# Kernel optimization log

Measured on AMD Instinct MI355X. Metric: run time of the kernel, lower is better.

The kernel has to match this reference:

```python
import jax, jax.numpy as jnp
import numpy as np

B, N, C, H, MLP = 4, 1024, 768, 6, 2304  # num_heads = C // 128
D = C // H  # head dim = 128


def setup_inputs() -> dict:
    key = jax.random.key(0)
    ks = iter(jax.random.split(key, 64))
    def nrm(shape, s=0.02):
        return jax.random.normal(next(ks), shape, jnp.float32) * s
    inp = {}
    for nm in ("queries", "change_emb", "imageA_emb", "imageB_emb", "pe"):
        inp[nm] = jax.random.normal(next(ks), (B, N, C), jnp.float32)
    # three Attention modules: self-attn (1), change->ABC cross (2), imageAB->change cross (3)
    for i in (1, 2, 3):
        for p in ("q", "k", "v", "o"):
            inp[f"w{p}{i}"] = nrm((C, C))       # stored [in, out]; y = x @ W + b
            inp[f"b{p}{i}"] = jnp.zeros((C,), jnp.float32)
    for i in (1, 2, 3):
        inp[f"ln{i}_w"] = jnp.ones((C,), jnp.float32)
        inp[f"ln{i}_b"] = jnp.zeros((C,), jnp.float32)
    inp["mlp_w1"] = nrm((C, MLP)); inp["mlp_b1"] = jnp.zeros((MLP,), jnp.float32)
    inp["mlp_w2"] = nrm((MLP, C)); inp["mlp_b2"] = jnp.zeros((C,), jnp.float32)
    inp["flag_a"] = nrm((C,)); inp["flag_b"] = nrm((C,)); inp["flag_c"] = nrm((C,))
    return inp


def _ln(x, w, b, eps=1e-5):
    m = jnp.mean(x, -1, keepdims=True)
    v = jnp.var(x, -1, keepdims=True)
    return (x - m) * jax.lax.rsqrt(v + eps) * w + b


def _mha(q, k, v, wq, bq, wk, bk, wv, bv, wo, bo):
    b, nq, _ = q.shape
    qh = (q @ wq + bq).reshape(b, nq, H, D)
    kh = (k @ wk + bk).reshape(b, k.shape[1], H, D)
    vh = (v @ wv + bv).reshape(b, v.shape[1], H, D)
    scores = jnp.einsum('bqhd,bkhd->bhqk', qh, kh) / np.float32(np.sqrt(D))
    attn = jax.nn.softmax(scores, axis=-1)
    out = jnp.einsum('bhqk,bkhd->bqhd', attn, vh).reshape(b, nq, H * D)
    return out @ wo + bo


def reference(queries, change_emb, imageA_emb, imageB_emb, pe,
              wq1, bq1, wk1, bk1, wv1, bv1, wo1, bo1,
              wq2, bq2, wk2, bk2, wv2, bv2, wo2, bo2,
              wq3, bq3, wk3, bk3, wv3, bv3, wo3, bo3,
              ln1_w, ln1_b, ln2_w, ln2_b, ln3_w, ln3_b,
              mlp_w1, mlp_b1, mlp_w2, mlp_b2,
              flag_a, flag_b, flag_c):
    # --- self attention on change queries (skip_first_layer_add=False) ---
    q0 = queries + change_emb
    a = _mha(q0 + pe, q0 + pe, q0, wq1, bq1, wk1, bk1, wv1, bv1, wo1, bo1)
    q1 = _ln(q0 + a, ln1_w, ln1_b)
    # --- cross attention: change -> [imageA, imageB, change] ---
    qf = q1 + pe + flag_c
    k2 = jnp.concatenate((imageA_emb + pe + flag_a,
                          imageB_emb + pe + flag_b,
                          q1 + pe + flag_c), axis=1)
    v2 = jnp.concatenate((imageA_emb, imageB_emb, q1), axis=1)
    a = _mha(qf, k2, v2, wq2, bq2, wk2, bk2, wv2, bv2, wo2, bo2)
    q2 = _ln(q1 + a, ln2_w, ln2_b)
    # --- MLP (exact GELU, as nn.GELU default) ---
    mlp_out = jax.nn.gelu(q2 @ mlp_w1 + mlp_b1, approximate=False) @ mlp_w2 + mlp_b2
    q3 = _ln(q2 + mlp_out, ln3_w, ln3_b)
    change_out = q3
    # --- cross attention: [imageA; imageB] -> [image; change], batched along dim 0 ---
    qa = imageA_emb + pe + flag_a
    qb = imageB_emb + pe + flag_b
    ka = jnp.concatenate((imageA_emb + pe + flag_a, q3 + pe + flag_c), axis=1)
    kb = jnp.concatenate((imageB_emb + pe + flag_b, q3 + pe + flag_c), axis=1)
    va = jnp.concatenate((imageA_emb, q3), axis=1)
    vb = jnp.concatenate((imageB_emb, q3), axis=1)
    q = jnp.concatenate((qa, qb), axis=0)   # [2B, N, C]
    k = jnp.concatenate((ka, kb), axis=0)   # [2B, 2N, C]
    v = jnp.concatenate((va, vb), axis=0)
    a = _mha(q, k, v, wq3, bq3, wk3, bk3, wv3, bv3, wo3, bo3)
    q = q + a
    image_A_refined, image_B_refined = jnp.split(q, 2, axis=0)
    return (image_A_refined, image_B_refined, change_out)
```

## Files before the change

kernel.cpp:

```cpp
#include <hip/hip_runtime.h>
#include <hip/hip_bf16.h>
#include <math.h>

typedef short bf16x8 __attribute__((ext_vector_type(8)));
typedef float f32x4 __attribute__((ext_vector_type(4)));
using bf16_t = __hip_bfloat16;

#define DEV static __device__ __forceinline__

DEV unsigned short f2bu(float x) {
  bf16_t h = __float2bfloat16(x);
  unsigned short u;
  __builtin_memcpy(&u, &h, 2);
  return u;
}
DEV void st4(bf16_t* p, float a, float b, float c, float d) {
  ushort4 u;
  u.x = f2bu(a); u.y = f2bu(b); u.z = f2bu(c); u.w = f2bu(d);
  *reinterpret_cast<ushort4*>(p) = u;
}

DEV void async_copy16(const bf16_t* g, bf16_t* lds) {
  __builtin_amdgcn_global_load_lds(
      (const __attribute__((address_space(1))) unsigned int*)g,
      (__attribute__((address_space(3))) unsigned int*)lds, 16, 0, 0);
}

struct WPack {
  const float* s[12];
  bf16_t* d[12];
  float scale0;
};

__global__ __launch_bounds__(256) void k_wt12(WPack pk) {
  __shared__ float tile[32][33];
  int z = blockIdx.z;
  const float* W = pk.s[z];
  bf16_t* WT = pk.d[z];
  float scale = (z == 0) ? pk.scale0 : 1.0f;
  int i0 = blockIdx.x * 32;
  int o0 = blockIdx.y * 32;
  int tx = threadIdx.x & 31, ty = threadIdx.x >> 5;
  for (int r = ty; r < 32; r += 8)
    tile[r][tx] = W[(size_t)(i0 + r) * 768 + (o0 + tx)];
  __syncthreads();
  for (int r = ty; r < 32; r += 8)
    WT[(size_t)(o0 + r) * 768 + (i0 + tx)] = __float2bfloat16(tile[tx][r] * scale);
}

__global__ __launch_bounds__(256) void k_wt(const float* __restrict__ W, bf16_t* __restrict__ WT,
                                            int in_dim, int out_dim) {
  __shared__ float tile[32][33];
  int i0 = blockIdx.x * 32;
  int o0 = blockIdx.y * 32;
  int tx = threadIdx.x & 31, ty = threadIdx.x >> 5;
  for (int r = ty; r < 32; r += 8)
    tile[r][tx] = W[(size_t)(i0 + r) * out_dim + (o0 + tx)];
  __syncthreads();
  for (int r = ty; r < 32; r += 8)
    WT[(size_t)(o0 + r) * in_dim + (i0 + tx)] = __float2bfloat16(tile[tx][r]);
}

__global__ __launch_bounds__(256) void k_bqk(const float* __restrict__ bq, const float* __restrict__ bk,
                                             float* __restrict__ out, float qa) {
  int i = blockIdx.x * 256 + threadIdx.x;
  if (i < 768) out[i] = bq[i] * qa;
  else if (i < 1536) out[i] = bk[i - 768];
}

__global__ __launch_bounds__(256) void k_prep1(const float4* __restrict__ q, const float4* __restrict__ ce,
                                               const float4* __restrict__ pe,
                                               bf16_t* __restrict__ qpe_b, bf16_t* __restrict__ q0_b, int n4) {
  int i = blockIdx.x * 256 + threadIdx.x;
  if (i >= n4) return;
  float4 a = q[i], b = ce[i], p = pe[i];
  float sx = a.x + b.x, sy = a.y + b.y, sz = a.z + b.z, sw = a.w + b.w;
  st4(q0_b + 4 * (size_t)i, sx, sy, sz, sw);
  st4(qpe_b + 4 * (size_t)i, sx + p.x, sy + p.y, sz + p.z, sw + p.w);
}

__global__ __launch_bounds__(256) void k_buildqq(const float* __restrict__ imA, const float* __restrict__ imB,
                                                 const float* __restrict__ pe, const float* __restrict__ fa,
                                                 const float* __restrict__ fb, bf16_t* __restrict__ qq,
                                                 bf16_t* __restrict__ imAB) {
  int idx = blockIdx.x * 256 + threadIdx.x;
  int c4 = idx % 192; int rem = idx / 192;
  int n = rem & 1023; int bb = rem >> 10;
  int b = bb & 3, isB = bb >> 2;
  int c = c4 * 4;
  size_t tok = (size_t)(b * 1024 + n) * 768 + c;
  float4 s = *(const float4*)((isB ? imB : imA) + tok);
  float4 p = *(const float4*)(pe + tok);
  float4 f = *(const float4*)((isB ? fb : fa) + c);
  size_t o = (size_t)rem * 768 + c;
  st4(imAB + o, s.x, s.y, s.z, s.w);
  st4(qq + o, s.x + p.x + f.x, s.y + p.y + f.y, s.z + p.z + f.z, s.w + p.w + f.w);
}

struct FArgs {
  const bf16_t* Q; bf16_t* O;
  const bf16_t* Kp[3]; const bf16_t* Vp[3];
  int badd[3], bmask[3];
  int ldq, ldk;
  long qStrideB, oStrideB;
};

template<int NSEG>
__global__ __launch_bounds__(256, 3) void k_flash(FArgs fa) {
  const int z = blockIdx.y; const int b = z / 6, h = z % 6;
  const bf16_t* Qb = fa.Q + (size_t)b * fa.qStrideB + h * 128;
  bf16_t* Ob = fa.O + (size_t)b * fa.oStrideB + h * 128;
  const int q0 = blockIdx.x * 64;
  const int tid = threadIdx.x, lane = tid & 63, w = tid >> 6;
  const int g = lane >> 4, c = lane & 15;

  __shared__ bf16_t Ks[64][136];
  __shared__ bf16_t Vs[128][72];
  __shared__ bf16_t Ps[64][72];

  bf16x8 qf[4];
#pragma unroll
  for (int kk = 0; kk < 4; kk++)
    qf[kk] = *reinterpret_cast<const bf16x8*>(
        &Qb[(size_t)(q0 + w * 16 + c) * fa.ldq + kk * 32 + g * 8]);

  f32x4 oa[8];
  float m[4], l[4];
#pragma unroll
  for (int d = 0; d < 8; d++) { f32x4 zz = {0.f, 0.f, 0.f, 0.f}; oa[d] = zz; }
#pragma unroll
  for (int r = 0; r < 4; r++) { m[r] = -1.0e30f; l[r] = 0.f; }

  const int kr_ = tid >> 4, kc_ = (tid & 15) * 8;
  const int vr_ = tid >> 3, vc_ = (tid & 7) * 8;
  const int ldk = fa.ldk;

#pragma unroll
  for (int s = 0; s < NSEG; ++s) {
    const int bi = fa.badd[s] + (b & fa.bmask[s]);
    const bf16_t* Kb = fa.Kp[s] + (size_t)bi * 1024 * ldk + h * 128;
    const bf16_t* Vb = fa.Vp[s] + (size_t)(bi * 6 + h) * 128 * 1024;
    for (int t = 0; t < 16; ++t) {
      const int k0 = t << 6;
#pragma unroll
      for (int p = 0; p < 4; p++)
        *reinterpret_cast<uint4*>(&Ks[p * 16 + kr_][kc_]) =
            *reinterpret_cast<const uint4*>(&Kb[(size_t)(k0 + p * 16 + kr_) * ldk + kc_]);
#pragma unroll
      for (int p = 0; p < 4; p++)
        *reinterpret_cast<uint4*>(&Vs[p * 32 + vr_][vc_]) =
            *reinterpret_cast<const uint4*>(&Vb[(size_t)(p * 32 + vr_) * 1024 + k0 + vc_]);
      __syncthreads();

      f32x4 sx[4];
#pragma unroll
      for (int j = 0; j < 4; j++) { f32x4 zz = {0.f, 0.f, 0.f, 0.f}; sx[j] = zz; }
      __builtin_amdgcn_s_setprio(1);
#pragma unroll
      for (int kk = 0; kk < 4; kk++)
#pragma unroll
        for (int j = 0; j < 4; j++) {
          bf16x8 kf = *reinterpret_cast<const bf16x8*>(&Ks[j * 16 + c][kk * 32 + g * 8]);
          sx[j] = __builtin_amdgcn_mfma_f32_16x16x32_bf16(qf[kk], kf, sx[j], 0, 0, 0);
        }
      __builtin_amdgcn_s_setprio(0);

      float tl[4];
#pragma unroll
      for (int r = 0; r < 4; r++)
        tl[r] = fmaxf(fmaxf(sx[0][r], sx[1][r]), fmaxf(sx[2][r], sx[3][r]));
      float ex = fmaxf(fmaxf(tl[0] - m[0], tl[1] - m[1]), fmaxf(tl[2] - m[2], tl[3] - m[3]));
      if (__any(ex > 8.0f)) {
#pragma unroll
        for (int r = 0; r < 4; r++) {
          float tv = tl[r];
          tv = fmaxf(tv, __shfl_xor(tv, 1));
          tv = fmaxf(tv, __shfl_xor(tv, 2));
          tv = fmaxf(tv, __shfl_xor(tv, 4));
          tv = fmaxf(tv, __shfl_xor(tv, 8));
          float mn = fmaxf(m[r], tv);
          float f = exp2f(m[r] - mn);
          m[r] = mn;
          l[r] *= f;
#pragma unroll
          for (int d = 0; d < 8; d++) oa[d][r] *= f;
        }
      }
#pragma unroll
      for (int j = 0; j < 4; j++)
#pragma unroll
        for (int r = 0; r < 4; r++) {
          float p = exp2f(sx[j][r] - m[r]);
          l[r] += p;
          Ps[w * 16 + g * 4 + r][j * 16 + c] = __float2bfloat16(p);
        }

      __builtin_amdgcn_s_setprio(1);
#pragma unroll
      for (int kk = 0; kk < 2; kk++) {
        bf16x8 pf = *reinterpret_cast<const bf16x8*>(&Ps[w * 16 + c][kk * 32 + g * 8]);
#pragma unroll
        for (int d = 0; d < 8; d++) {
          bf16x8 vf = *reinterpret_cast<const bf16x8*>(&Vs[d * 16 + c][kk * 32 + g * 8]);
          oa[d] = __builtin_amdgcn_mfma_f32_16x16x32_bf16(pf, vf, oa[d], 0, 0, 0);
        }
      }
      __builtin_amdgcn_s_setprio(0);
      __syncthreads();
    }
  }

  float inv[4];
#pragma unroll
  for (int r = 0; r < 4; r++) {
    float t2 = l[r];
    t2 += __shfl_xor(t2, 1);
    t2 += __shfl_xor(t2, 2);
    t2 += __shfl_xor(t2, 4);
    t2 += __shfl_xor(t2, 8);
    inv[r] = 1.0f / t2;
  }
#pragma unroll
  for (int d = 0; d < 8; d++) {
    int col = d * 16 + c;
#pragma unroll
    for (int r = 0; r < 4; r++) {
      int row = q0 + w * 16 + g * 4 + r;
      Ob[(size_t)row * 768 + col] = __float2bfloat16(oa[d][r] * inv[r]);
    }
  }
}

__global__ __launch_bounds__(256) void k_ln(const float* __restrict__ X1, const float* __restrict__ X2,
                                            const float* __restrict__ A,
                                            const float* __restrict__ w, const float* __restrict__ bvec,
                                            float* __restrict__ outf, bf16_t* __restrict__ outb,
                                            const float* __restrict__ pe, const float* __restrict__ flag,
                                            bf16_t* __restrict__ outpf) {
  int row = blockIdx.x, tid = threadIdx.x;
  size_t base = (size_t)row * 768;
  float v0 = X1[base + tid] + A[base + tid];
  float v1 = X1[base + tid + 256] + A[base + tid + 256];
  float v2 = X1[base + tid + 512] + A[base + tid + 512];
  if (X2) {
    v0 += X2[base + tid]; v1 += X2[base + tid + 256]; v2 += X2[base + tid + 512];
  }
  float s = v0 + v1 + v2;
  for (int o = 32; o; o >>= 1) s += __shfl_xor(s, o);
  __shared__ float sm[8];
  int wv = tid >> 6, ln = tid & 63;
  if (ln == 0) sm[wv] = s;
  __syncthreads();
  s = sm[0] + sm[1] + sm[2] + sm[3];
  float mean = s * (1.0f / 768.0f);
  float d0 = v0 - mean, d1 = v1 - mean, d2 = v2 - mean;
  float ss = d0 * d0 + d1 * d1 + d2 * d2;
  for (int o = 32; o; o >>= 1) ss += __shfl_xor(ss, o);
  if (ln == 0) sm[4 + wv] = ss;
  __syncthreads();
  ss = sm[4] + sm[5] + sm[6] + sm[7];
  float rstd = rsqrtf(ss * (1.0f / 768.0f) + 1e-5f);
  float o0 = d0 * rstd * w[tid] + bvec[tid];
  float o1 = d1 * rstd * w[tid + 256] + bvec[tid + 256];
  float o2 = d2 * rstd * w[tid + 512] + bvec[tid + 512];
  outf[base + tid] = o0; outf[base + tid + 256] = o1; outf[base + tid + 512] = o2;
  if (outb) {
    outb[base + tid] = __float2bfloat16(o0);
    outb[base + tid + 256] = __float2bfloat16(o1);
    outb[base + tid + 512] = __float2bfloat16(o2);
  }
  if (outpf) {
    outpf[base + tid] = __float2bfloat16(o0 + pe[base + tid] + flag[tid]);
    outpf[base + tid + 256] = __float2bfloat16(o1 + pe[base + tid + 256] + flag[tid + 256]);
    outpf[base + tid + 512] = __float2bfloat16(o2 + pe[base + tid + 512] + flag[tid + 512]);
  }
}

struct GArgs {
  const bf16_t* X; const bf16_t* Wt; const float* bias; void* Out;
  const bf16_t* resid;
  int K, ldx, ldw, ldo, vNk, mode;
  float alpha;
};
struct GPack {
  GArgs a[7];
  int cum[7];
  int nx[7];
};

__global__ __launch_bounds__(256, 2) void k_gemmN(GPack pk) {
  GArgs a; int base, nx;
  {
    int idx = blockIdx.x;
    if (idx < pk.cum[0])      { a = pk.a[0]; base = 0;          nx = pk.nx[0]; }
    else if (idx < pk.cum[1]) { a = pk.a[1]; base = pk.cum[0];  nx = pk.nx[1]; }
    else if (idx < pk.cum[2]) { a = pk.a[2]; base = pk.cum[1];  nx = pk.nx[2]; }
    else if (idx < pk.cum[3]) { a = pk.a[3]; base = pk.cum[2];  nx = pk.nx[3]; }
    else if (idx < pk.cum[4]) { a = pk.a[4]; base = pk.cum[3];  nx = pk.nx[4]; }
    else if (idx < pk.cum[5]) { a = pk.a[5]; base = pk.cum[4];  nx = pk.nx[5]; }
    else                      { a = pk.a[6]; base = pk.cum[5];  nx = pk.nx[6]; }
  }
  int idx = blockIdx.x - base;
  const int brow = (idx / nx) * 128;
  const int bcol = (idx % nx) * 128;

  __shared__ bf16_t As[128 * 32];
  __shared__ bf16_t Bs[128 * 32];

  const int tid = threadIdx.x;
  const int lane = tid & 63;
  const int wave = tid >> 6;
  const int wr = wave >> 1;
  const int wc = wave & 1;

  f32x4 acc[4][4];
#pragma unroll
  for (int i = 0; i < 4; i++)
#pragma unroll
    for (int j = 0; j < 4; j++) {
      f32x4 zz = {0.f, 0.f, 0.f, 0.f};
      acc[i][j] = zz;
    }

  const int sr = lane >> 2;
  const int sc = (lane & 3) * 8;
  const int lrow = lane & 15;
  const int kch = (lane >> 4) * 8;

  const int nK = a.K >> 5;
  for (int kk = 0; kk < nK; ++kk) {
    const int k0 = kk << 5;
#pragma unroll
    for (int q = 0; q < 2; q++) {
      const int rows = wave * 32 + q * 16;
      async_copy16(a.X + (size_t)(brow + rows + sr) * a.ldx + k0 + sc, As + rows * 32);
      async_copy16(a.Wt + (size_t)(bcol + rows + sr) * a.ldw + k0 + sc, Bs + rows * 32);
    }
    __syncthreads();

    bf16x8 afr[4], bfr[4];
#pragma unroll
    for (int i = 0; i < 4; i++)
      afr[i] = *reinterpret_cast<const bf16x8*>(&As[(wr * 64 + i * 16 + lrow) * 32 + kch]);
#pragma unroll
    for (int j = 0; j < 4; j++)
      bfr[j] = *reinterpret_cast<const bf16x8*>(&Bs[(wc * 64 + j * 16 + lrow) * 32 + kch]);
#pragma unroll
    for (int i = 0; i < 4; i++)
#pragma unroll
      for (int j = 0; j < 4; j++)
        acc[i][j] = __builtin_amdgcn_mfma_f32_16x16x32_bf16(afr[i], bfr[j], acc[i][j], 0, 0, 0);
    __syncthreads();
  }

  const int lcol = lane & 15;
  const int lrow4 = (lane >> 4) * 4;

  if (a.mode == 2) {
    const int bi = brow / a.vNk;
    const int n0 = brow - bi * a.vNk;
#pragma unroll
    for (int i = 0; i < 4; i++) {
      int rloc = n0 + wr * 64 + i * 16 + lrow4;
#pragma unroll
      for (int j = 0; j < 4; j++) {
        int col = bcol + wc * 64 + j * 16 + lcol;
        int hh = col >> 7, dd = col & 127;
        float bv = a.bias[col];
        ushort4 u;
        u.x = f2bu(acc[i][j][0] + bv);
        u.y = f2bu(acc[i][j][1] + bv);
        u.z = f2bu(acc[i][j][2] + bv);
        u.w = f2bu(acc[i][j][3] + bv);
        bf16_t* dst = reinterpret_cast<bf16_t*>(a.Out) +
                      ((size_t)(bi * 6 + hh) * 128 + dd) * (size_t)a.vNk + rloc;
        *reinterpret_cast<ushort4*>(dst) = u;
      }
    }
  } else if (a.mode == 3) {
#pragma unroll
    for (int i = 0; i < 4; i++) {
      int row0 = brow + wr * 64 + i * 16 + lrow4;
#pragma unroll
      for (int j = 0; j < 4; j++) {
        int col = bcol + wc * 64 + j * 16 + lcol;
        float bv = a.bias[col];
#pragma unroll
        for (int r = 0; r < 4; r++) {
          size_t idx2 = (size_t)(row0 + r) * a.ldo + col;
          float rv = __bfloat162float(a.resid[(size_t)(row0 + r) * 768 + col]);
          reinterpret_cast<float*>(a.Out)[idx2] = acc[i][j][r] + bv + rv;
        }
      }
    }
  } else {
#pragma unroll
    for (int i = 0; i < 4; i++) {
      int row0 = brow + wr * 64 + i * 16 + lrow4;
#pragma unroll
      for (int j = 0; j < 4; j++) {
        int col = bcol + wc * 64 + j * 16 + lcol;
        float bv = a.bias[col];
#pragma unroll
        for (int r = 0; r < 4; r++)
          reinterpret_cast<bf16_t*>(a.Out)[(size_t)(row0 + r) * a.ldo + col] =
              __float2bfloat16((acc[i][j][r] + bv) * a.alpha);
      }
    }
  }
}

static inline void packN(hipStream_t st, const GArgs* as, const int* Ms, const int* Ns, int n) {
  GPack pk;
  int tot = 0;
  for (int i = 0; i < 7; ++i) {
    int j = i < n ? i : n - 1;
    pk.a[i] = as[j];
    pk.nx[i] = Ns[j] / 128;
    if (i < n) tot += (Ns[j] / 128) * (Ms[j] / 128);
    pk.cum[i] = tot;
  }
  k_gemmN<<<dim3(tot), 256, 0, st>>>(pk);
}

template<int OUTBF, int GELU>
__global__ __launch_bounds__(256, 2) void k_gemm(
    const bf16_t* __restrict__ X, const bf16_t* __restrict__ Wt,
    const float* __restrict__ bias, void* __restrict__ Out,
    int M, int Nout, int K, int ldx, int ldw, int ldo, float alpha) {
  const int brow = blockIdx.y * 128;
  const int bcol = blockIdx.x * 128;

  __shared__ bf16_t As[128 * 32];
  __shared__ bf16_t Bs[128 * 32];

  const int tid = threadIdx.x;
  const int lane = tid & 63;
  const int wave = tid >> 6;
  const int wr = wave >> 1;
  const int wc = wave & 1;

  f32x4 acc[4][4];
#pragma unroll
  for (int i = 0; i < 4; i++)
#pragma unroll
    for (int j = 0; j < 4; j++) {
      f32x4 zz = {0.f, 0.f, 0.f, 0.f};
      acc[i][j] = zz;
    }

  const int sr = lane >> 2;
  const int sc = (lane & 3) * 8;
  const int lrow = lane & 15;
  const int kch = (lane >> 4) * 8;

  const int nK = K >> 5;
  for (int kk = 0; kk < nK; ++kk) {
    const int k0 = kk << 5;
#pragma unroll
    for (int q = 0; q < 2; q++) {
      const int rows = wave * 32 + q * 16;
      async_copy16(X + (size_t)(brow + rows + sr) * ldx + k0 + sc, As + rows * 32);
      async_copy16(Wt + (size_t)(bcol + rows + sr) * ldw + k0 + sc, Bs + rows * 32);
    }
    __syncthreads();

    bf16x8 afr[4], bfr[4];
#pragma unroll
    for (int i = 0; i < 4; i++)
      afr[i] = *reinterpret_cast<const bf16x8*>(&As[(wr * 64 + i * 16 + lrow) * 32 + kch]);
#pragma unroll
    for (int j = 0; j < 4; j++)
      bfr[j] = *reinterpret_cast<const bf16x8*>(&Bs[(wc * 64 + j * 16 + lrow) * 32 + kch]);
#pragma unroll
    for (int i = 0; i < 4; i++)
#pragma unroll
      for (int j = 0; j < 4; j++)
        acc[i][j] = __builtin_amdgcn_mfma_f32_16x16x32_bf16(afr[i], bfr[j], acc[i][j], 0, 0, 0);
    __syncthreads();
  }

  const int lcol = lane & 15;
  const int lrow4 = (lane >> 4) * 4;

#pragma unroll
  for (int i = 0; i < 4; i++) {
    int row0 = brow + wr * 64 + i * 16 + lrow4;
#pragma unroll
    for (int j = 0; j < 4; j++) {
      int col = bcol + wc * 64 + j * 16 + lcol;
      float bv = bias ? bias[col] : 0.0f;
#pragma unroll
      for (int r = 0; r < 4; r++) {
        float v = (acc[i][j][r] + bv) * alpha;
        if (GELU) v = 0.5f * v * (1.0f + erff(v * 0.70710678118f));
        size_t idx = (size_t)(row0 + r) * ldo + col;
        if (OUTBF) reinterpret_cast<bf16_t*>(Out)[idx] = __float2bfloat16(v);
        else reinterpret_cast<float*>(Out)[idx] = v;
      }
    }
  }
}

static inline void gemm(hipStream_t st, const bf16_t* X, const bf16_t* Wt, const float* bias,
                        void* out, int outBf, int gelu, int M, int N, int K,
                        int ldx, int ldw, int ldo, float alpha = 1.0f) {
  dim3 g(N / 128, M / 128), blk(256);
  if (outBf) {
    if (gelu) k_gemm<1, 1><<<g, blk, 0, st>>>(X, Wt, bias, out, M, N, K, ldx, ldw, ldo, alpha);
    else      k_gemm<1, 0><<<g, blk, 0, st>>>(X, Wt, bias, out, M, N, K, ldx, ldw, ldo, alpha);
  } else      k_gemm<0, 0><<<g, blk, 0, st>>>(X, Wt, bias, out, M, N, K, ldx, ldw, ldo, alpha);
}

extern "C" void kernel_launch(void* const* d_in, const int* in_sizes, int n_in,
                              void* d_out, int out_size, void* d_ws, size_t ws_size,
                              hipStream_t stream) {
  (void)in_sizes; (void)n_in; (void)out_size; (void)ws_size;
  constexpr int B = 4, N = 1024, C = 768, Hh = 6, MLPD = 2304;
  constexpr size_t BNC = (size_t)B * N * C;
  constexpr size_t NC  = (size_t)N * C;
  const float qalpha = 0.08838834764831845f * 1.4426950408889634f;

  const float* queries = (const float*)d_in[0];
  const float* change  = (const float*)d_in[1];
  const float* imA     = (const float*)d_in[2];
  const float* imB     = (const float*)d_in[3];
  const float* pe      = (const float*)d_in[4];
  const float* bq1 = (const float*)d_in[6];  const float* bk1 = (const float*)d_in[8];
  const float* bv1 = (const float*)d_in[10]; const float* bo1 = (const float*)d_in[12];
  const float* bq2 = (const float*)d_in[14]; const float* bk2 = (const float*)d_in[16];
  const float* bv2 = (const float*)d_in[18]; const float* bo2 = (const float*)d_in[20];
  const float* bq3 = (const float*)d_in[22]; const float* bk3 = (const float*)d_in[24];
  const float* bv3 = (const float*)d_in[26]; const float* bo3 = (const float*)d_in[28];
  const float* ln1w = (const float*)d_in[29]; const float* ln1b = (const float*)d_in[30];
  const float* ln2w = (const float*)d_in[31]; const float* ln2b = (const float*)d_in[32];
  const float* ln3w = (const float*)d_in[33]; const float* ln3b = (const float*)d_in[34];
  const float* mb1 = (const float*)d_in[36]; const float* mb2 = (const float*)d_in[38];
  const float* fa = (const float*)d_in[39];
  const float* fb = (const float*)d_in[40];
  const float* fc = (const float*)d_in[41];

  char* base = (char*)d_ws;
  size_t off = 0;
  auto alloc = [&](size_t bytes) -> void* {
    void* p = base + off;
    off += (bytes + 255) & ~(size_t)255;
    return p;
  };

  bf16_t* WT[14];
  const int widx[14] = {5, 7, 9, 11, 13, 15, 17, 19, 21, 23, 25, 27, 35, 37};
  for (int i = 0; i < 12; i++) WT[i] = (bf16_t*)alloc((size_t)768 * 768 * 2);
  WT[12] = (bf16_t*)alloc((size_t)768 * 2304 * 2);
  WT[13] = (bf16_t*)alloc((size_t)2304 * 768 * 2);
  float* bqk1 = (float*)alloc(1536 * 4);
  float*  q1  = (float*)alloc(BNC * 4);
  float*  q2  = (float*)alloc(BNC * 4);
  bf16_t* q2b = (bf16_t*)alloc(BNC * 2);
  bf16_t* q1b = (bf16_t*)alloc(BNC * 2);
  bf16_t* qq   = (bf16_t*)alloc(2 * BNC * 2);
  bf16_t* Q3h  = (bf16_t*)alloc(2 * BNC * 2);
  bf16_t* K2i  = (bf16_t*)alloc(2 * BNC * 2);
  bf16_t* vT2i = (bf16_t*)alloc(2 * BNC * 2);
  bf16_t* K3i  = (bf16_t*)alloc(2 * BNC * 2);
  bf16_t* vT3i = (bf16_t*)alloc(2 * BNC * 2);
  const size_t arena = off;

  float* dof = (float*)d_out;
  float* chg = dof + 2 * BNC;

  WPack pk;
  for (int i = 0; i < 12; i++) { pk.s[i] = (const float*)d_in[widx[i]]; pk.d[i] = WT[i]; }
  pk.scale0 = qalpha;
  k_wt12<<<dim3(24, 24, 12), 256, 0, stream>>>(pk);
  k_wt<<<dim3(24, 72), 256, 0, stream>>>((const float*)d_in[35], WT[12], 768, 2304);
  k_wt<<<dim3(72, 24), 256, 0, stream>>>((const float*)d_in[37], WT[13], 2304, 768);
  k_bqk<<<dim3(6), 256, 0, stream>>>(bq1, bk1, bqk1, qalpha);

  off = arena;
  bf16_t* qpe_b = (bf16_t*)alloc(BNC * 2);
  bf16_t* q0_b  = (bf16_t*)alloc(BNC * 2);
  bf16_t* imAB  = (bf16_t*)alloc(2 * BNC * 2);
  bf16_t* QKh   = (bf16_t*)alloc((size_t)B * N * 1536 * 2);
  bf16_t* vT1   = (bf16_t*)alloc(BNC * 2);
  bf16_t* attC  = (bf16_t*)alloc(BNC * 2);
  float*  a1    = dof;

  k_prep1<<<dim3((int)(BNC / 4 / 256)), 256, 0, stream>>>(
      (const float4*)queries, (const float4*)change, (const float4*)pe, qpe_b, q0_b, (int)(BNC / 4));
  k_buildqq<<<dim3((int)(2 * BNC / 4 / 256)), 256, 0, stream>>>(imA, imB, pe, fa, fb, qq, imAB);
  {
    GArgs as[7] = {
      {qpe_b, WT[0], bqk1, QKh,  nullptr, C, C, C, 1536, 0,    1, 1.0f},
      {q0_b,  WT[2], bv1,  vT1,  nullptr, C, C, C, 0,    1024, 2, 1.0f},
      {qq,    WT[8], bq3,  Q3h,  nullptr, C, C, C, C,    0,    1, qalpha},
      {qq,    WT[5], bk2,  K2i,  nullptr, C, C, C, C,    0,    1, 1.0f},
      {imAB,  WT[6], bv2,  vT2i, nullptr, C, C, C, 0,    1024, 2, 1.0f},
      {qq,    WT[9], bk3,  K3i,  nullptr, C, C, C, C,    0,    1, 1.0f},
      {imAB,  WT[10],bv3,  vT3i, nullptr, C, C, C, 0,    1024, 2, 1.0f},
    };
    int Ms[7] = {B * N, B * N, 2 * B * N, 2 * B * N, 2 * B * N, 2 * B * N, 2 * B * N};
    int Ns[7] = {1536, C, C, C, C, C, C};
    packN(stream, as, Ms, Ns, 7);
  }
  {
    FArgs f1 = {QKh, attC, {QKh + 768, QKh + 768, QKh + 768}, {vT1, vT1, vT1},
                {0, 0, 0}, {7, 7, 7}, 1536, 1536, (long)N * 1536, (long)NC};
    k_flash<1><<<dim3(16, B * Hh), 256, 0, stream>>>(f1);
  }
  gemm(stream, attC, WT[3], bo1, a1, 0, 0, B * N, C, C, C, C, C);
  k_ln<<<dim3(B * N), 256, 0, stream>>>(queries, change, a1, ln1w, ln1b, q1, q1b, pe, fc, nullptr);

  off = arena;
  bf16_t* qf    = (bf16_t*)alloc(BNC * 2);
  bf16_t* Q2h   = (bf16_t*)alloc(BNC * 2);
  bf16_t* K2c   = (bf16_t*)alloc(BNC * 2);
  bf16_t* vT2c  = (bf16_t*)alloc(BNC * 2);
  bf16_t* attC2 = (bf16_t*)alloc(BNC * 2);
  float*  a2    = dof;

  {
    struct L {
      static __global__ void run(const float* q1_, const float* pe_, const float* fc_,
                                 bf16_t* qf_) {
        int idx = blockIdx.x * 256 + threadIdx.x;
        int c = (idx % 192) * 4;
        size_t tok = (size_t)idx * 4;
        float4 xv = *(const float4*)(q1_ + tok);
        float4 p = *(const float4*)(pe_ + tok);
        float4 f = *(const float4*)(fc_ + c);
        st4(qf_ + tok, xv.x + p.x + f.x, xv.y + p.y + f.y, xv.z + p.z + f.z, xv.w + p.w + f.w);
      }
    };
    L::run<<<dim3((int)(BNC / 4 / 256)), 256, 0, stream>>>(q1, pe, fc, qf);
  }
  {
    GArgs as[3] = {
      {qf,  WT[4], bq2, Q2h,  nullptr, C, C, C, C, 0,    1, qalpha},
      {qf,  WT[5], bk2, K2c,  nullptr, C, C, C, C, 0,    1, 1.0f},
      {q1b, WT[6], bv2, vT2c, nullptr, C, C, C, 0, 1024, 2, 1.0f},
    };
    int Ms[3] = {B * N, B * N, B * N};
    int Ns[3] = {C, C, C};
    packN(stream, as, Ms, Ns, 3);
  }
  {
    FArgs f2 = {Q2h, attC2, {K2i, K2i, K2c}, {vT2i, vT2i, vT2c},
                {0, 4, 0}, {3, 3, 3}, C, C, (long)NC, (long)NC};
    k_flash<3><<<dim3(16, B * Hh), 256, 0, stream>>>(f2);
  }
  gemm(stream, attC2, WT[7], bo2, a2, 0, 0, B * N, C, C, C, C, C);
  k_ln<<<dim3(B * N), 256, 0, stream>>>(q1, (const float*)nullptr, a2, ln2w, ln2b, q2, q2b,
                                        (const float*)nullptr, (const float*)nullptr, (bf16_t*)nullptr);

  off = arena;
  bf16_t* h1 = (bf16_t*)alloc((size_t)B * N * MLPD * 2);
  float*  a3 = dof;
  gemm(stream, q2b, WT[12], mb1, h1, 1, 1, B * N, MLPD, C, C, C, MLPD);
  gemm(stream, h1, WT[13], mb2, a3, 0, 0, B * N, C, MLPD, MLPD, MLPD, C);

  off = arena;
  bf16_t* cf    = (bf16_t*)alloc(BNC * 2);
  bf16_t* chgb  = (bf16_t*)alloc(BNC * 2);
  bf16_t* K3c   = (bf16_t*)alloc(BNC * 2);
  bf16_t* vT3c  = (bf16_t*)alloc(BNC * 2);
  bf16_t* attC3 = (bf16_t*)alloc(2 * BNC * 2);

  k_ln<<<dim3(B * N), 256, 0, stream>>>(q2, (const float*)nullptr, a3, ln3w, ln3b, chg, chgb,
                                        pe, fc, cf);
  {
    GArgs as[2] = {
      {cf,   WT[9],  bk3, K3c,  nullptr, C, C, C, C, 0,    1, 1.0f},
      {chgb, WT[10], bv3, vT3c, nullptr, C, C, C, 0, 1024, 2, 1.0f},
    };
    int Ms[2] = {B * N, B * N};
    int Ns[2] = {C, C};
    packN(stream, as, Ms, Ns, 2);
  }
  {
    FArgs f3 = {Q3h, attC3, {K3i, K3c, K3c}, {vT3i, vT3c, vT3c},
                {0, 0, 0}, {7, 3, 3}, C, C, (long)NC, (long)NC};
    k_flash<2><<<dim3(16, 2 * B * Hh), 256, 0, stream>>>(f3);
  }
  {
    GArgs as[1] = {{attC3, WT[11], bo3, dof, qq, C, C, C, C, 0, 3, 1.0f}};
    int Ms[1] = {2 * B * N};
    int Ns[1] = {C};
    packN(stream, as, Ms, Ns, 1);
  }
}
```

Before: 642.3 us.

## Merge same-input projection GEMMs into wide GEMMs with segmented output pointers

```diff
diff --git a/kernel.cpp b/kernel.cpp
--- a/kernel.cpp
+++ b/kernel.cpp
@@ -27,17 +27,17 @@
 }
 
 struct WPack {
-  const float* s[12];
-  bf16_t* d[12];
-  float scale0;
+  const float* s[13];
+  bf16_t* d[13];
+  float scale[13];
 };
 
-__global__ __launch_bounds__(256) void k_wt12(WPack pk) {
+__global__ __launch_bounds__(256) void k_wt13(WPack pk) {
   __shared__ float tile[32][33];
   int z = blockIdx.z;
   const float* W = pk.s[z];
   bf16_t* WT = pk.d[z];
-  float scale = (z == 0) ? pk.scale0 : 1.0f;
+  float scale = pk.scale[z];
   int i0 = blockIdx.x * 32;
   int o0 = blockIdx.y * 32;
   int tx = threadIdx.x & 31, ty = threadIdx.x >> 5;
@@ -61,11 +61,14 @@
     WT[(size_t)(o0 + r) * in_dim + (i0 + tx)] = __float2bfloat16(tile[tx][r]);
 }
 
-__global__ __launch_bounds__(256) void k_bqk(const float* __restrict__ bq, const float* __restrict__ bk,
-                                             float* __restrict__ out, float qa) {
+__global__ __launch_bounds__(256) void k_bcat(const float* __restrict__ s0, const float* __restrict__ s1,
+                                              const float* __restrict__ s2, float a0,
+                                              float* __restrict__ out, int nseg) {
   int i = blockIdx.x * 256 + threadIdx.x;
-  if (i < 768) out[i] = bq[i] * qa;
-  else if (i < 1536) out[i] = bk[i - 768];
+  if (i >= nseg * 768) return;
+  int seg = i / 768, c = i - seg * 768;
+  const float* s = seg == 0 ? s0 : (seg == 1 ? s1 : s2);
+  out[i] = s[c] * (seg == 0 ? a0 : 1.0f);
 }
 
 __global__ __launch_bounds__(256) void k_prep1(const float4* __restrict__ q, const float4* __restrict__ ce,
@@ -277,10 +280,10 @@
 }
 
 struct GArgs {
-  const bf16_t* X; const bf16_t* Wt; const float* bias; void* Out;
+  const bf16_t* X; const bf16_t* Wt; const float* bias;
+  void* O0; void* O1; void* O2;
   const bf16_t* resid;
   int K, ldx, ldw, ldo, vNk, mode;
-  float alpha;
 };
 struct GPack {
   GArgs a[7];
@@ -289,18 +292,18 @@
 };
 
 __global__ __launch_bounds__(256, 2) void k_gemmN(GPack pk) {
-  GArgs a; int base, nx;
+  GArgs a; int gbase, nx;
   {
     int idx = blockIdx.x;
-    if (idx < pk.cum[0])      { a = pk.a[0]; base = 0;          nx = pk.nx[0]; }
-    else if (idx < pk.cum[1]) { a = pk.a[1]; base = pk.cum[0];  nx = pk.nx[1]; }
-    else if (idx < pk.cum[2]) { a = pk.a[2]; base = pk.cum[1];  nx = pk.nx[2]; }
-    else if (idx < pk.cum[3]) { a = pk.a[3]; base = pk.cum[2];  nx = pk.nx[3]; }
-    else if (idx < pk.cum[4]) { a = pk.a[4]; base = pk.cum[3];  nx = pk.nx[4]; }
-    else if (idx < pk.cum[5]) { a = pk.a[5]; base = pk.cum[4];  nx = pk.nx[5]; }
-    else                      { a = pk.a[6]; base = pk.cum[5];  nx = pk.nx[6]; }
-  }
-  int idx = blockIdx.x - base;
+    if (idx < pk.cum[0])      { a = pk.a[0]; gbase = 0;          nx = pk.nx[0]; }
+    else if (idx < pk.cum[1]) { a = pk.a[1]; gbase = pk.cum[0];  nx = pk.nx[1]; }
+    else if (idx < pk.cum[2]) { a = pk.a[2]; gbase = pk.cum[1];  nx = pk.nx[2]; }
+    else if (idx < pk.cum[3]) { a = pk.a[3]; gbase = pk.cum[2];  nx = pk.nx[3]; }
+    else if (idx < pk.cum[4]) { a = pk.a[4]; gbase = pk.cum[3];  nx = pk.nx[4]; }
+    else if (idx < pk.cum[5]) { a = pk.a[5]; gbase = pk.cum[4];  nx = pk.nx[5]; }
+    else                      { a = pk.a[6]; gbase = pk.cum[5];  nx = pk.nx[6]; }
+  }
+  int idx = blockIdx.x - gbase;
   const int brow = (idx / nx) * 128;
   const int bcol = (idx % nx) * 128;
 
@@ -356,6 +359,11 @@
   const int lcol = lane & 15;
   const int lrow4 = (lane >> 4) * 4;
 
+  int seg = 0;
+  if (a.O1) seg = bcol / 768;
+  void* ob = seg == 0 ? a.O0 : (seg == 1 ? a.O1 : a.O2);
+  const int cofs = seg * 768;
+
   if (a.mode == 2) {
     const int bi = brow / a.vNk;
     const int n0 = brow - bi * a.vNk;
@@ -364,15 +372,16 @@
       int rloc = n0 + wr * 64 + i * 16 + lrow4;
 #pragma unroll
       for (int j = 0; j < 4; j++) {
-        int col = bcol + wc * 64 + j * 16 + lcol;
+        int colf = bcol + wc * 64 + j * 16 + lcol;
+        int col = colf - cofs;
         int hh = col >> 7, dd = col & 127;
-        float bv = a.bias[col];
+        float bv = a.bias[colf];
         ushort4 u;
         u.x = f2bu(acc[i][j][0] + bv);
         u.y = f2bu(acc[i][j][1] + bv);
         u.z = f2bu(acc[i][j][2] + bv);
         u.w = f2bu(acc[i][j][3] + bv);
-        bf16_t* dst = reinterpret_cast<bf16_t*>(a.Out) +
+        bf16_t* dst = reinterpret_cast<bf16_t*>(ob) +
                       ((size_t)(bi * 6 + hh) * 128 + dd) * (size_t)a.vNk + rloc;
         *reinterpret_cast<ushort4*>(dst) = u;
       }
@@ -389,7 +398,7 @@
         for (int r = 0; r < 4; r++) {
           size_t idx2 = (size_t)(row0 + r) * a.ldo + col;
           float rv = __bfloat162float(a.resid[(size_t)(row0 + r) * 768 + col]);
-          reinterpret_cast<float*>(a.Out)[idx2] = acc[i][j][r] + bv + rv;
+          reinterpret_cast<float*>(a.O0)[idx2] = acc[i][j][r] + bv + rv;
         }
       }
     }
@@ -399,12 +408,13 @@
       int row0 = brow + wr * 64 + i * 16 + lrow4;
 #pragma unroll
       for (int j = 0; j < 4; j++) {
-        int col = bcol + wc * 64 + j * 16 + lcol;
-        float bv = a.bias[col];
+        int colf = bcol + wc * 64 + j * 16 + lcol;
+        int col = colf - cofs;
+        float bv = a.bias[colf];
 #pragma unroll
         for (int r = 0; r < 4; r++)
-          reinterpret_cast<bf16_t*>(a.Out)[(size_t)(row0 + r) * a.ldo + col] =
-              __float2bfloat16((acc[i][j][r] + bv) * a.alpha);
+          reinterpret_cast<bf16_t*>(ob)[(size_t)(row0 + r) * a.ldo + col] =
+              __float2bfloat16(acc[i][j][r] + bv);
       }
     }
   }
@@ -548,16 +558,31 @@
     return p;
   };
 
-  bf16_t* WT[14];
-  const int widx[14] = {5, 7, 9, 11, 13, 15, 17, 19, 21, 23, 25, 27, 35, 37};
-  for (int i = 0; i < 12; i++) WT[i] = (bf16_t*)alloc((size_t)768 * 768 * 2);
-  WT[12] = (bf16_t*)alloc((size_t)768 * 2304 * 2);
-  WT[13] = (bf16_t*)alloc((size_t)2304 * 768 * 2);
-  float* bqk1 = (float*)alloc(1536 * 4);
+  bf16_t* WT[12]; bf16_t* WT5b; bf16_t* WTm1; bf16_t* WTm2;
+  WT[0] = (bf16_t*)alloc((size_t)768 * 768 * 2);
+  WT[1] = (bf16_t*)alloc((size_t)768 * 768 * 2);
+  WT[2] = (bf16_t*)alloc((size_t)768 * 768 * 2);
+  WT[3] = (bf16_t*)alloc((size_t)768 * 768 * 2);
+  WT[8] = (bf16_t*)alloc((size_t)768 * 768 * 2);
+  WT[5] = (bf16_t*)alloc((size_t)768 * 768 * 2);
+  WT[9] = (bf16_t*)alloc((size_t)768 * 768 * 2);
+  WT[6] = (bf16_t*)alloc((size_t)768 * 768 * 2);
+  WT[10] = (bf16_t*)alloc((size_t)768 * 768 * 2);
+  WT[4] = (bf16_t*)alloc((size_t)768 * 768 * 2);
+  WT5b  = (bf16_t*)alloc((size_t)768 * 768 * 2);
+  WT[7] = (bf16_t*)alloc((size_t)768 * 768 * 2);
+  WT[11] = (bf16_t*)alloc((size_t)768 * 768 * 2);
+  WTm1 = (bf16_t*)alloc((size_t)768 * 2304 * 2);
+  WTm2 = (bf16_t*)alloc((size_t)2304 * 768 * 2);
+  float* bqk1  = (float*)alloc(1536 * 4);
+  float* bKm   = (float*)alloc(2304 * 4);
+  float* bVm   = (float*)alloc(1536 * 4);
+  float* bQ2K2 = (float*)alloc(1536 * 4);
   float*  q1  = (float*)alloc(BNC * 4);
   float*  q2  = (float*)alloc(BNC * 4);
   bf16_t* q2b = (bf16_t*)alloc(BNC * 2);
   bf16_t* q1b = (bf16_t*)alloc(BNC * 2);
+  bf16_t* qf  = (bf16_t*)alloc(BNC * 2);
   bf16_t* qq   = (bf16_t*)alloc(2 * BNC * 2);
   bf16_t* Q3h  = (bf16_t*)alloc(2 * BNC * 2);
   bf16_t* K2i  = (bf16_t*)alloc(2 * BNC * 2);
@@ -569,13 +594,23 @@
   float* dof = (float*)d_out;
   float* chg = dof + 2 * BNC;
 
-  WPack pk;
-  for (int i = 0; i < 12; i++) { pk.s[i] = (const float*)d_in[widx[i]]; pk.d[i] = WT[i]; }
-  pk.scale0 = qalpha;
-  k_wt12<<<dim3(24, 24, 12), 256, 0, stream>>>(pk);
-  k_wt<<<dim3(24, 72), 256, 0, stream>>>((const float*)d_in[35], WT[12], 768, 2304);
-  k_wt<<<dim3(72, 24), 256, 0, stream>>>((const float*)d_in[37], WT[13], 2304, 768);
-  k_bqk<<<dim3(6), 256, 0, stream>>>(bq1, bk1, bqk1, qalpha);
+  {
+    WPack pk;
+    const int widx[12] = {5, 7, 9, 11, 13, 15, 17, 19, 21, 23, 25, 27};
+    for (int i = 0; i < 12; i++) {
+      pk.s[i] = (const float*)d_in[widx[i]];
+      pk.d[i] = WT[i];
+      pk.scale[i] = (i == 0 || i == 4 || i == 8) ? qalpha : 1.0f;
+    }
+    pk.s[12] = (const float*)d_in[15]; pk.d[12] = WT5b; pk.scale[12] = 1.0f;
+    k_wt13<<<dim3(24, 24, 13), 256, 0, stream>>>(pk);
+  }
+  k_wt<<<dim3(24, 72), 256, 0, stream>>>((const float*)d_in[35], WTm1, 768, 2304);
+  k_wt<<<dim3(72, 24), 256, 0, stream>>>((const float*)d_in[37], WTm2, 2304, 768);
+  k_bcat<<<dim3(6), 256, 0, stream>>>(bq1, bk1, nullptr, qalpha, bqk1, 2);
+  k_bcat<<<dim3(9), 256, 0, stream>>>(bq3, bk2, bk3, qalpha, bKm, 3);
+  k_bcat<<<dim3(6), 256, 0, stream>>>(bv2, bv3, nullptr, 1.0f, bVm, 2);
+  k_bcat<<<dim3(6), 256, 0, stream>>>(bq2, bk2, nullptr, qalpha, bQ2K2, 2);
 
   off = arena;
   bf16_t* qpe_b = (bf16_t*)alloc(BNC * 2);
@@ -590,18 +625,15 @@
       (const float4*)queries, (const float4*)change, (const float4*)pe, qpe_b, q0_b, (int)(BNC / 4));
   k_buildqq<<<dim3((int)(2 * BNC / 4 / 256)), 256, 0, stream>>>(imA, imB, pe, fa, fb, qq, imAB);
   {
-    GArgs as[7] = {
-      {qpe_b, WT[0], bqk1, QKh,  nullptr, C, C, C, 1536, 0,    1, 1.0f},
-      {q0_b,  WT[2], bv1,  vT1,  nullptr, C, C, C, 0,    1024, 2, 1.0f},
-      {qq,    WT[8], bq3,  Q3h,  nullptr, C, C, C, C,    0,    1, qalpha},
-      {qq,    WT[5], bk2,  K2i,  nullptr, C, C, C, C,    0,    1, 1.0f},
-      {imAB,  WT[6], bv2,  vT2i, nullptr, C, C, C, 0,    1024, 2, 1.0f},
-      {qq,    WT[9], bk3,  K3i,  nullptr, C, C, C, C,    0,    1, 1.0f},
-      {imAB,  WT[10],bv3,  vT3i, nullptr, C, C, C, 0,    1024, 2, 1.0f},
+    GArgs as[4] = {
+      {qpe_b, WT[0], bqk1, QKh,  nullptr, nullptr, nullptr, C, C, C, 1536, 0,    1},
+      {q0_b,  WT[2], bv1,  vT1,  nullptr, nullptr, nullptr, C, C, C, 0,    1024, 2},
+      {qq,    WT[8], bKm,  Q3h,  K2i,     K3i,     nullptr, C, C, C, 768,  0,    1},
+      {imAB,  WT[6], bVm,  vT2i, vT3i,    nullptr, nullptr, C, C, C, 0,    1024, 2},
     };
-    int Ms[7] = {B * N, B * N, 2 * B * N, 2 * B * N, 2 * B * N, 2 * B * N, 2 * B * N};
-    int Ns[7] = {1536, C, C, C, C, C, C};
-    packN(stream, as, Ms, Ns, 7);
+    int Ms[4] = {B * N, B * N, 2 * B * N, 2 * B * N};
+    int Ns[4] = {1536, C, 2304, 1536};
+    packN(stream, as, Ms, Ns, 4);
   }
   {
     FArgs f1 = {QKh, attC, {QKh + 768, QKh + 768, QKh + 768}, {vT1, vT1, vT1},
@@ -609,10 +641,9 @@
     k_flash<1><<<dim3(16, B * Hh), 256, 0, stream>>>(f1);
   }
   gemm(stream, attC, WT[3], bo1, a1, 0, 0, B * N, C, C, C, C, C);
-  k_ln<<<dim3(B * N), 256, 0, stream>>>(queries, change, a1, ln1w, ln1b, q1, q1b, pe, fc, nullptr);
+  k_ln<<<dim3(B * N), 256, 0, stream>>>(queries, change, a1, ln1w, ln1b, q1, q1b, pe, fc, qf);
 
   off = arena;
-  bf16_t* qf    = (bf16_t*)alloc(BNC * 2);
   bf16_t* Q2h   = (bf16_t*)alloc(BNC * 2);
   bf16_t* K2c   = (bf16_t*)alloc(BNC * 2);
   bf16_t* vT2c  = (bf16_t*)alloc(BNC * 2);
@@ -620,29 +651,13 @@
   float*  a2    = dof;
 
   {
-    struct L {
-      static __global__ void run(const float* q1_, const float* pe_, const float* fc_,
-                                 bf16_t* qf_) {
-        int idx = blockIdx.x * 256 + threadIdx.x;
-        int c = (idx % 192) * 4;
-        size_t tok = (size_t)idx * 4;
-        float4 xv = *(const float4*)(q1_ + tok);
-        float4 p = *(const float4*)(pe_ + tok);
-        float4 f = *(const float4*)(fc_ + c);
-        st4(qf_ + tok, xv.x + p.x + f.x, xv.y + p.y + f.y, xv.z + p.z + f.z, xv.w + p.w + f.w);
-      }
+    GArgs as[2] = {
+      {qf,  WT[4], bQ2K2, Q2h,  K2c,    nullptr, nullptr, C, C, C, 768,  0,    1},
+      {q1b, WT[6], bv2,   vT2c, nullptr, nullptr, nullptr, C, C, C, 0,    1024, 2},
     };
-    L::run<<<dim3((int)(BNC / 4 / 256)), 256, 0, stream>>>(q1, pe, fc, qf);
-  }
-  {
-    GArgs as[3] = {
-      {qf,  WT[4], bq2, Q2h,  nullptr, C, C, C, C, 0,    1, qalpha},
-      {qf,  WT[5], bk2, K2c,  nullptr, C, C, C, C, 0,    1, 1.0f},
-      {q1b, WT[6], bv2, vT2c, nullptr, C, C, C, 0, 1024, 2, 1.0f},
-    };
-    int Ms[3] = {B * N, B * N, B * N};
-    int Ns[3] = {C, C, C};
-    packN(stream, as, Ms, Ns, 3);
+    int Ms[2] = {B * N, B * N};
+    int Ns[2] = {1536, C};
+    packN(stream, as, Ms, Ns, 2);
   }
   {
     FArgs f2 = {Q2h, attC2, {K2i, K2i, K2c}, {vT2i, vT2i, vT2c},
@@ -656,8 +671,8 @@
   off = arena;
   bf16_t* h1 = (bf16_t*)alloc((size_t)B * N * MLPD * 2);
   float*  a3 = dof;
-  gemm(stream, q2b, WT[12], mb1, h1, 1, 1, B * N, MLPD, C, C, C, MLPD);
-  gemm(stream, h1, WT[13], mb2, a3, 0, 0, B * N, C, MLPD, MLPD, MLPD, C);
+  gemm(stream, q2b, WTm1, mb1, h1, 1, 1, B * N, MLPD, C, C, C, MLPD);
+  gemm(stream, h1, WTm2, mb2, a3, 0, 0, B * N, C, MLPD, MLPD, MLPD, C);
 
   off = arena;
   bf16_t* cf    = (bf16_t*)alloc(BNC * 2);
@@ -670,8 +685,8 @@
                                         pe, fc, cf);
   {
     GArgs as[2] = {
-      {cf,   WT[9],  bk3, K3c,  nullptr, C, C, C, C, 0,    1, 1.0f},
-      {chgb, WT[10], bv3, vT3c, nullptr, C, C, C, 0, 1024, 2, 1.0f},
+      {cf,   WT[9],  bk3, K3c,  nullptr, nullptr, nullptr, C, C, C, 768,  0,    1},
+      {chgb, WT[10], bv3, vT3c, nullptr, nullptr, nullptr, C, C, C, 0,    1024, 2},
     };
     int Ms[2] = {B * N, B * N};
     int Ns[2] = {C, C};
@@ -683,7 +698,7 @@
     k_flash<2><<<dim3(16, 2 * B * Hh), 256, 0, stream>>>(f3);
   }
   {
-    GArgs as[1] = {{attC3, WT[11], bo3, dof, qq, C, C, C, C, 0, 3, 1.0f}};
+    GArgs as[1] = {{attC3, WT[11], bo3, dof, nullptr, nullptr, qq, C, C, C, C, 0, 3}};
     int Ms[1] = {2 * B * N};
     int Ns[1] = {C};
     packN(stream, as, Ms, Ns, 1);
```

After: 638.5 us. Within noise of the previous version (-0.6%).
